# Kernel optimization log

Measured on AMD Instinct MI355X. Metric: run time of the kernel, lower is better.

## Reference

```python
import jax, jax.numpy as jnp
import numpy as np

IN_C, OUT_C, K, STRIDE, PAD = 64, 128, 3, 1, 1


def setup_inputs() -> dict:
    key = jax.random.key(0)
    kx, kw = jax.random.split(key)
    x = jax.random.normal(kx, (16, IN_C, 112, 112), dtype=jnp.float32)
    scale = np.sqrt(2.0 / (IN_C * K * K)).astype(np.float32)
    weight = jax.random.normal(kw, (OUT_C, IN_C, K, K), dtype=jnp.float32) * scale
    bias = jnp.zeros((OUT_C,), dtype=jnp.float32)
    return {"x": x, "weight": weight, "bias": bias}


def reference(x, weight, bias):
    # Direct 2D convolution (cross-correlation, like torch Conv2d), NCHW layout.
    out = jax.lax.conv_general_dilated(
        x, weight,
        window_strides=(STRIDE, STRIDE),
        padding=((PAD, PAD), (PAD, PAD)),
        dimension_numbers=("NCHW", "OIHW", "NCHW"),
    )
    return out + bias[None, :, None, None]
```

## Files before the change

### kernel.cpp

```cpp
#include <hip/hip_runtime.h>
#include <stdint.h>


#define HW     112
#define PIX    12544
#define ICN    64
#define OCN    128
#define TILEP  128
#define PTILES 98
#define NBLK   1568
#define NIMG   16

#define XT_BYTES   (NIMG * PIX * ICN * 2)
#define WT_OFF     XT_BYTES
#define WT_BYTES   (9 * OCN * ICN * 2)
#define ZG_OFF     (WT_OFF + WT_BYTES)
#define XBLK       (NIMG * (PIX / 64))
#define WBLK       72

#define XU_LO      113
#define XU_DATA    354
#define XU_ZROW    354
#define XU_ROWS    355

typedef __attribute__((ext_vector_type(8))) __bf16 bf16x8;
typedef __attribute__((ext_vector_type(4))) float  f32x4;

__device__ __forceinline__ uint32_t rne_lo(float f) {
    uint32_t u = __builtin_bit_cast(uint32_t, f);
    return (u + 0x7fffu + ((u >> 16) & 1u)) >> 16;
}
__device__ __forceinline__ uint32_t pk2(float a, float b) {
    uint32_t ub = __builtin_bit_cast(uint32_t, b);
    ub = (ub + 0x7fffu + ((ub >> 16) & 1u)) & 0xffff0000u;
    return rne_lo(a) | ub;
}

__device__ __forceinline__ void load_lds16(const void* g, void* l) {
    __builtin_amdgcn_global_load_lds(
        (const __attribute__((address_space(1))) uint32_t*)g,
        (__attribute__((address_space(3))) uint32_t*)l, 16, 0, 0);
}

__global__ void __launch_bounds__(256)
prep(const float* __restrict__ x, const float* __restrict__ w, uint8_t* __restrict__ ws) {
    const int b = blockIdx.x;
    const int t = threadIdx.x;
    uint16_t* xt = (uint16_t*)ws;
    uint16_t* wt = (uint16_t*)(ws + WT_OFF);

    if (b < XBLK) {
        const int n  = b / (PIX / 64);
        const int p0 = (b - n * (PIX / 64)) * 64;
        const int px = t >> 2;
        const int q  = t & 3;
        const float* src = x + ((size_t)n * ICN + q * 16) * PIX + p0 + px;
        float v[16];
#pragma unroll
        for (int i = 0; i < 16; ++i) v[i] = src[(size_t)i * PIX];
        uint4 u0 = make_uint4(pk2(v[0], v[1]),  pk2(v[2], v[3]),
                              pk2(v[4], v[5]),  pk2(v[6], v[7]));
        uint4 u1 = make_uint4(pk2(v[8], v[9]),  pk2(v[10], v[11]),
                              pk2(v[12], v[13]), pk2(v[14], v[15]));
        char* dst = (char*)xt + ((size_t)(n * PIX + p0 + px)) * 128 + q * 32;
        *(uint4*)dst        = u0;
        *(uint4*)(dst + 16) = u1;
    } else {
        const int wb = b - XBLK;
#pragma unroll
        for (int k = 0; k < 4; ++k) {
            int wi = wb * 1024 + k * 256 + t;
            int r  = wi >> 13;
            int oc = (wi >> 6) & 127;
            int ic = wi & 63;
            wt[wi] = (uint16_t)rne_lo(w[oc * 576 + ic * 9 + r]);
        }
        if (wb == 0 && t < 8) ((uint4*)(ws + ZG_OFF))[t] = make_uint4(0, 0, 0, 0);
    }
}

__global__ void __launch_bounds__(256)
conv_mfma(const uint8_t* __restrict__ ws, const float* __restrict__ bias,
          float* __restrict__ out) {
    __shared__ uint8_t Wb[2][16384];
    __shared__ uint8_t Xu[XU_ROWS * 128];

    const char* xt = (const char*)ws;
    const char* wt = (const char*)(ws + WT_OFF);
    const char* zg = (const char*)(ws + ZG_OFF);

    const int t = threadIdx.x;
    const int b = blockIdx.x;
    const int n_img = b / PTILES;
    const int p0 = (b - n_img * PTILES) * TILEP;

    const int lane = t & 63;
    const int wave = t >> 6;
    const int lr = lane & 15;
    const int lq = lane >> 4;
    const int oc_base = (wave & 1) * 64;
    const int px_base = (wave >> 1) * 64;

    const int rowB  = t >> 3;
    const int cswz8 = ((t & 7) ^ (rowB & 7)) * 16;
    const char* zaddr = zg + (t & 7) * 16;

    const char* xrow0 = xt + ((ptrdiff_t)(n_img * PIX + p0 - XU_LO)) * 128 + cswz8;
#pragma unroll
    for (int r2 = 0; r2 < 11; ++r2) {
        int r = r2 * 32 + rowB;
        int p = p0 - XU_LO + r;
        const char* gp = ((unsigned)p < PIX) ? (xrow0 + (ptrdiff_t)r * 128) : zaddr;
        load_lds16(gp, (char*)Xu + r2 * 4096 + wave * 1024);
    }
    if (t < 16) {
        int r = 352 + (t >> 3);
        int p = p0 - XU_LO + r;
        const char* gp = ((unsigned)p < PIX) ? (xrow0 + (ptrdiff_t)r * 128) : zaddr;
        load_lds16(gp, (char*)Xu + 352 * 128);
    }
    if (t < 8) *(uint4*)((char*)Xu + XU_ZROW * 128 + t * 16) = make_uint4(0, 0, 0, 0);

    const char* wsrc = wt + rowB * 128 + cswz8;
#pragma unroll
    for (int r2 = 0; r2 < 4; ++r2)
        load_lds16(wsrc + r2 * 4096, (char*)Wb + r2 * 4096 + wave * 1024);

    int hh[4], wwp[4], rb[4];
#pragma unroll
    for (int ni = 0; ni < 4; ++ni) {
        int p = p0 + px_base + ni * 16 + lr;
        int h = p / HW;
        hh[ni]  = h;
        wwp[ni] = p - h * HW;
        rb[ni]  = px_base + ni * 16 + lr + XU_LO;
    }

    f32x4 acc[4][4];
    {
        f32x4 z = {0.f, 0.f, 0.f, 0.f};
#pragma unroll
        for (int i = 0; i < 4; ++i)
#pragma unroll
            for (int j = 0; j < 4; ++j) acc[i][j] = z;
    }

    __syncthreads();

#pragma unroll
    for (int tap = 0; tap < 9; ++tap) {
        const int dy = tap / 3 - 1;
        const int dx = tap - (tap / 3) * 3 - 1;
        const int roff = dy * HW + dx;

        if (tap < 8) {
#pragma unroll
            for (int r2 = 0; r2 < 4; ++r2)
                load_lds16(wsrc + (tap + 1) * 16384 + r2 * 4096,
                           (char*)Wb + ((tap + 1) & 1) * 16384 + r2 * 4096 + wave * 1024);
        }

        int ro[4];
#pragma unroll
        for (int ni = 0; ni < 4; ++ni) {
            bool ok = ((unsigned)(hh[ni] + dy) < HW) & ((unsigned)(wwp[ni] + dx) < HW);
            ro[ni] = ok ? (rb[ni] + roff) : XU_ZROW;
        }

        const char* wbase = (const char*)Wb + (tap & 1) * 16384;
#pragma unroll
        for (int kh = 0; kh < 2; ++kh) {
            const int cc = kh * 4 + lq;
            bf16x8 a_frag[4], b_frag[4];
#pragma unroll
            for (int mi = 0; mi < 4; ++mi) {
                int R = oc_base + mi * 16 + lr;
                a_frag[mi] = *(const bf16x8*)(wbase + R * 128 + ((cc ^ (R & 7)) * 16));
            }
#pragma unroll
            for (int ni = 0; ni < 4; ++ni)
                b_frag[ni] = *(const bf16x8*)((const char*)Xu + ro[ni] * 128
                                              + ((cc ^ (ro[ni] & 7)) * 16));
#pragma unroll
            for (int mi = 0; mi < 4; ++mi)
#pragma unroll
                for (int ni = 0; ni < 4; ++ni)
                    acc[mi][ni] = __builtin_amdgcn_mfma_f32_16x16x32_bf16(
                        a_frag[mi], b_frag[ni], acc[mi][ni], 0, 0, 0);
        }
        if (tap < 8) __syncthreads();
    }

#pragma unroll
    for (int mi = 0; mi < 4; ++mi) {
#pragma unroll
        for (int rg = 0; rg < 4; ++rg) {
            const int oc = oc_base + mi * 16 + lq * 4 + rg;
            const float bb = bias[oc];
            float* orow = out + ((size_t)n_img * OCN + oc) * PIX + p0 + px_base + lr;
#pragma unroll
            for (int ni = 0; ni < 4; ++ni)
                orow[ni * 16] = acc[mi][ni][rg] + bb;
        }
    }
}

extern "C" void kernel_launch(void* const* d_in, const int* in_sizes, int n_in,
                              void* d_out, int out_size, void* d_ws, size_t ws_size,
                              hipStream_t stream) {
    const float* x    = (const float*)d_in[0];
    const float* w    = (const float*)d_in[1];
    const float* bias = (const float*)d_in[2];
    float* out = (float*)d_out;
    uint8_t* ws = (uint8_t*)d_ws;

    prep<<<XBLK + WBLK, 256, 0, stream>>>(x, w, ws);
    conv_mfma<<<NBLK, 256, 0, stream>>>(ws, bias, out);
}
```

Baseline: 179.6 us.

## Read conv input fragments directly from global memory instead of LDS halo tile

Measured after the change: 218.2 us. +21.5%, slower.

```diff
diff --git a/kernel.cpp b/kernel.cpp
--- a/kernel.cpp
+++ b/kernel.cpp
@@ -17,11 +17,6 @@
 #define ZG_OFF     (WT_OFF + WT_BYTES)
 #define XBLK       (NIMG * (PIX / 64))
 #define WBLK       72
-
-#define XU_LO      113
-#define XU_DATA    354
-#define XU_ZROW    354
-#define XU_ROWS    355
 
 typedef __attribute__((ext_vector_type(8))) __bf16 bf16x8;
 typedef __attribute__((ext_vector_type(4))) float  f32x4;
@@ -79,11 +74,10 @@
     }
 }
 
-__global__ void __launch_bounds__(256)
+__global__ void __launch_bounds__(256, 4)
 conv_mfma(const uint8_t* __restrict__ ws, const float* __restrict__ bias,
           float* __restrict__ out) {
     __shared__ uint8_t Wb[2][16384];
-    __shared__ uint8_t Xu[XU_ROWS * 128];
 
     const char* xt = (const char*)ws;
     const char* wt = (const char*)(ws + WT_OFF);
@@ -103,38 +97,22 @@
 
     const int rowB  = t >> 3;
     const int cswz8 = ((t & 7) ^ (rowB & 7)) * 16;
-    const char* zaddr = zg + (t & 7) * 16;
-
-    const char* xrow0 = xt + ((ptrdiff_t)(n_img * PIX + p0 - XU_LO)) * 128 + cswz8;
-#pragma unroll
-    for (int r2 = 0; r2 < 11; ++r2) {
-        int r = r2 * 32 + rowB;
-        int p = p0 - XU_LO + r;
-        const char* gp = ((unsigned)p < PIX) ? (xrow0 + (ptrdiff_t)r * 128) : zaddr;
-        load_lds16(gp, (char*)Xu + r2 * 4096 + wave * 1024);
-    }
-    if (t < 16) {
-        int r = 352 + (t >> 3);
-        int p = p0 - XU_LO + r;
-        const char* gp = ((unsigned)p < PIX) ? (xrow0 + (ptrdiff_t)r * 128) : zaddr;
-        load_lds16(gp, (char*)Xu + 352 * 128);
-    }
-    if (t < 8) *(uint4*)((char*)Xu + XU_ZROW * 128 + t * 16) = make_uint4(0, 0, 0, 0);
-
     const char* wsrc = wt + rowB * 128 + cswz8;
-#pragma unroll
-    for (int r2 = 0; r2 < 4; ++r2)
-        load_lds16(wsrc + r2 * 4096, (char*)Wb + r2 * 4096 + wave * 1024);
-
-    int hh[4], wwp[4], rb[4];
+
+    int hh[4], wwp[4];
+    const char* xbase[4];
 #pragma unroll
     for (int ni = 0; ni < 4; ++ni) {
         int p = p0 + px_base + ni * 16 + lr;
         int h = p / HW;
         hh[ni]  = h;
         wwp[ni] = p - h * HW;
-        rb[ni]  = px_base + ni * 16 + lr + XU_LO;
-    }
+        xbase[ni] = xt + ((ptrdiff_t)(n_img * PIX + p)) * 128 + lq * 16;
+    }
+
+#pragma unroll
+    for (int r2 = 0; r2 < 4; ++r2)
+        load_lds16(wsrc + r2 * 4096, (char*)Wb + r2 * 4096 + wave * 1024);
 
     f32x4 acc[4][4];
     {
@@ -151,7 +129,19 @@
     for (int tap = 0; tap < 9; ++tap) {
         const int dy = tap / 3 - 1;
         const int dx = tap - (tap / 3) * 3 - 1;
-        const int roff = dy * HW + dx;
+        const int boff = (dy * HW + dx) * 128;
+
+        const char* bp[4];
+#pragma unroll
+        for (int ni = 0; ni < 4; ++ni) {
+            bool ok = ((unsigned)(hh[ni] + dy) < HW) & ((unsigned)(wwp[ni] + dx) < HW);
+            bp[ni] = ok ? (xbase[ni] + boff) : zg;
+        }
+
+        bf16x8 b0[4];
+#pragma unroll
+        for (int ni = 0; ni < 4; ++ni)
+            b0[ni] = *(const bf16x8*)(bp[ni]);
 
         if (tap < 8) {
 #pragma unroll
@@ -160,34 +150,44 @@
                            (char*)Wb + ((tap + 1) & 1) * 16384 + r2 * 4096 + wave * 1024);
         }
 
-        int ro[4];
-#pragma unroll
-        for (int ni = 0; ni < 4; ++ni) {
-            bool ok = ((unsigned)(hh[ni] + dy) < HW) & ((unsigned)(wwp[ni] + dx) < HW);
-            ro[ni] = ok ? (rb[ni] + roff) : XU_ZROW;
-        }
-
         const char* wbase = (const char*)Wb + (tap & 1) * 16384;
-#pragma unroll
-        for (int kh = 0; kh < 2; ++kh) {
-            const int cc = kh * 4 + lq;
-            bf16x8 a_frag[4], b_frag[4];
+
+        {
+            const int cc = lq;
+            bf16x8 a_frag[4];
 #pragma unroll
             for (int mi = 0; mi < 4; ++mi) {
                 int R = oc_base + mi * 16 + lr;
                 a_frag[mi] = *(const bf16x8*)(wbase + R * 128 + ((cc ^ (R & 7)) * 16));
             }
 #pragma unroll
-            for (int ni = 0; ni < 4; ++ni)
-                b_frag[ni] = *(const bf16x8*)((const char*)Xu + ro[ni] * 128
-                                              + ((cc ^ (ro[ni] & 7)) * 16));
-#pragma unroll
             for (int mi = 0; mi < 4; ++mi)
 #pragma unroll
                 for (int ni = 0; ni < 4; ++ni)
                     acc[mi][ni] = __builtin_amdgcn_mfma_f32_16x16x32_bf16(
-                        a_frag[mi], b_frag[ni], acc[mi][ni], 0, 0, 0);
-        }
+                        a_frag[mi], b0[ni], acc[mi][ni], 0, 0, 0);
+        }
+
+        {
+            bf16x8 b1[4];
+#pragma unroll
+            for (int ni = 0; ni < 4; ++ni)
+                b1[ni] = *(const bf16x8*)(bp[ni] + 64);
+            const int cc = 4 + lq;
+            bf16x8 a_frag[4];
+#pragma unroll
+            for (int mi = 0; mi < 4; ++mi) {
+                int R = oc_base + mi * 16 + lr;
+                a_frag[mi] = *(const bf16x8*)(wbase + R * 128 + ((cc ^ (R & 7)) * 16));
+            }
+#pragma unroll
+            for (int mi = 0; mi < 4; ++mi)
+#pragma unroll
+                for (int ni = 0; ni < 4; ++ni)
+                    acc[mi][ni] = __builtin_amdgcn_mfma_f32_16x16x32_bf16(
+                        a_frag[mi], b1[ni], acc[mi][ni], 0, 0, 0);
+        }
+
         if (tap < 8) __syncthreads();
     }
 
```
